# Performance work log

Hardware: AMD Instinct MI355X
Metric: run time of the kernel (lower is better)

The kernel has to match this reference:

```python
import jax, jax.numpy as jnp
import numpy as np

N, E = 50000, 600000
D_IN = 128; D_HID = 128; D_OUT = 128
HEADS = 4; HD = D_HID // HEADS  # per-head dim (32); also edge-encoder output dim
EDGE_DIM = 64


def _w(key, shape, scale=0.05):
    return jax.random.normal(key, shape, dtype=jnp.float32) * scale


def setup_inputs() -> dict:
    key = jax.random.key(0)
    ks = jax.random.split(key, 20)
    return {
        "x": jax.random.normal(ks[0], (N, D_IN), dtype=jnp.float32),
        "edge_index": jax.random.randint(ks[1], (2, E), 0, N),
        "edge_attr": jax.random.normal(ks[2], (E, EDGE_DIM), dtype=jnp.float32),
        # edge feature encoders: Linear(EDGE_DIM, HD), one per GNN layer
        "ew0": _w(ks[3], (EDGE_DIM, HD)), "eb0": jnp.zeros((HD,), jnp.float32),
        "ew1": _w(ks[4], (EDGE_DIM, HD)), "eb1": jnp.zeros((HD,), jnp.float32),
        # ordered-message-passing attention: Linear(dim, 1) per layer
        "ow0": _w(ks[5], (D_IN, 1)), "ob0": jnp.zeros((1,), jnp.float32),
        "ow1": _w(ks[6], (D_OUT, 1)), "ob1": jnp.zeros((1,), jnp.float32),
        # GATConv layer 0: in=D_IN, heads=HEADS, per-head out=HD, edge_dim=HD
        "g0_W": _w(ks[7], (D_IN, HEADS * HD)),
        "g0_as": _w(ks[8], (HEADS, HD)), "g0_ad": _w(ks[9], (HEADS, HD)),
        "g0_We": _w(ks[10], (HD, HEADS * HD)), "g0_ae": _w(ks[11], (HEADS, HD)),
        "g0_b": jnp.zeros((HEADS * HD,), jnp.float32),
        # GATConv layer 1 (final): in=HEADS*HD, heads=1, out=D_OUT, edge_dim=HD
        "g1_W": _w(ks[12], (HEADS * HD, D_OUT)),
        "g1_as": _w(ks[13], (1, D_OUT)), "g1_ad": _w(ks[14], (1, D_OUT)),
        "g1_We": _w(ks[15], (HD, D_OUT)), "g1_ae": _w(ks[16], (1, D_OUT)),
        "g1_b": jnp.zeros((D_OUT,), jnp.float32),
    }


def _gat_conv(x, src, dst, e_attr, W, a_src, a_dst, We, a_e, bias):
    """PyG GATConv with edge features, add_self_loops=True, fill_value='mean'."""
    H, C = a_src.shape
    n = x.shape[0]
    # self-loop edge_attr = per-dst mean of incoming edge_attr (PyG fill_value='mean')
    ones = jnp.ones((src.shape[0],), x.dtype)
    cnt = jax.ops.segment_sum(ones, dst, num_segments=n)
    loop_attr = jax.ops.segment_sum(e_attr, dst, num_segments=n) / jnp.maximum(cnt, 1.0)[:, None]
    loop = jnp.arange(n)
    src2 = jnp.concatenate([src, loop])
    dst2 = jnp.concatenate([dst, loop])
    ea2 = jnp.concatenate([e_attr, loop_attr], axis=0)  # [E+N, HD]
    xs = (x @ W).reshape(n, H, C)                       # [N, H, C]
    al_src = jnp.einsum('nhc,hc->nh', xs, a_src)
    al_dst = jnp.einsum('nhc,hc->nh', xs, a_dst)
    ee = (ea2 @ We).reshape(-1, H, C)                   # [E+N, H, C]
    al_e = jnp.einsum('ehc,hc->eh', ee, a_e)
    alpha = jax.nn.leaky_relu(al_src[src2] + al_dst[dst2] + al_e, 0.2)  # [E+N, H]
    # segment softmax over edges sharing a destination node
    mx = jax.ops.segment_max(alpha, dst2, num_segments=n)
    ex = jnp.exp(alpha - mx[dst2])
    den = jax.ops.segment_sum(ex, dst2, num_segments=n)
    coef = ex / (den[dst2] + 1e-16)
    out = jax.ops.segment_sum(xs[src2] * coef[..., None], dst2, num_segments=n)
    return out.reshape(n, H * C) + bias


def reference(x, edge_index, edge_attr, ew0, eb0, ew1, eb1, ow0, ob0, ow1, ob1,
              g0_W, g0_as, g0_ad, g0_We, g0_ae, g0_b,
              g1_W, g1_as, g1_ad, g1_We, g1_ae, g1_b):
    src, dst = edge_index[0], edge_index[1]
    original_x = x
    layers = [
        (ew0, eb0, ow0, ob0, g0_W, g0_as, g0_ad, g0_We, g0_ae, g0_b),
        (ew1, eb1, ow1, ob1, g1_W, g1_as, g1_ad, g1_We, g1_ae, g1_b),
    ]
    for i, (ew, eb, ow, ob, W, a_s, a_d, We, a_e, b) in enumerate(layers):
        te = jax.nn.relu(edge_attr @ ew + eb)            # [E, HD]
        score = (x @ ow + ob)[:, 0]                       # [N] order-attention scores
        te = te * jnp.exp(score)[src][:, None]            # ordered message weighting
        x_new = _gat_conv(x, src, dst, te, W, a_s, a_d, We, a_e, b)
        x = x_new + x if x.shape[-1] == x_new.shape[-1] else x_new
        if i < len(layers) - 1:
            x = jax.nn.relu(x)  # dropout p=0.0 in eval
    if original_x.shape[-1] == x.shape[-1]:
        x = x + original_x
    return x
```

## Files before the change

### kernel.cpp

```cpp
#include <hip/hip_runtime.h>
#include <math.h>

#define D 128
#define ED 64
#define HD 32

typedef short s16x8 __attribute__((ext_vector_type(8)));
typedef float f32x4 __attribute__((ext_vector_type(4)));

static __device__ inline unsigned short f2b(float f) {
  unsigned int u = __float_as_uint(f);
  unsigned int r = (u + 0x7fff + ((u >> 16) & 1)) >> 16;
  return (unsigned short)r;
}
static __device__ inline float b2f(unsigned short b) {
  return __uint_as_float(((unsigned int)b) << 16);
}

__global__ __launch_bounds__(256)
void count_prep_kernel(const int* __restrict__ dst, int* __restrict__ cnt, int E, int egrid,
                       const float* __restrict__ g0W, unsigned short* __restrict__ Wt0,
                       const float* __restrict__ g1W, unsigned short* __restrict__ Wt1,
                       const float* __restrict__ ew0, unsigned short* __restrict__ ewt0,
                       const float* __restrict__ ew1, unsigned short* __restrict__ ewt1,
                       const float* __restrict__ g0We, const float* __restrict__ g0ae,
                       float* __restrict__ M0,
                       const float* __restrict__ g1We, const float* __restrict__ g1ae,
                       float* __restrict__ M1) {
  int b = blockIdx.x, t = threadIdx.x;
  if (b < egrid) {
    int e = b * 256 + t;
    if (e < E) atomicAdd(&cnt[dst[e]], 1);
    return;
  }
  int pb = b - egrid;
  if (pb < 128) {
    const float* W = pb < 64 ? g0W : g1W;
    unsigned short* Wt = pb < 64 ? Wt0 : Wt1;
    int id = (pb & 63) * 256 + t;
    int nn = id >> 7, k = id & 127;
    Wt[id] = f2b(W[k * D + nn]);
  } else if (pb < 144) {
    const float* ew = pb < 136 ? ew0 : ew1;
    unsigned short* ewt = pb < 136 ? ewt0 : ewt1;
    int id = ((pb - 128) & 7) * 256 + t;
    if (id < HD * ED) {
      int i = id >> 6, k = id & 63;
      int ch = (i < 16) ? ((i >> 2) * 8 + (i & 3))
                        : (((i - 16) >> 2) * 8 + 4 + ((i - 16) & 3));
      ewt[id] = f2b(ew[k * HD + ch]);
    }
  } else if (pb == 144) {
    if (t < HD * 4) {
      int d = t >> 2, h = t & 3;
      float s = 0.f;
      for (int c = 0; c < 32; ++c) s += g0We[d * D + h * 32 + c] * g0ae[h * 32 + c];
      M0[t] = s;
    }
  } else {
    if (t < HD) {
      float s = 0.f;
      for (int c = 0; c < D; ++c) s += g1We[t * D + c] * g1ae[c];
      M1[t] = s;
    }
  }
}

__global__ __launch_bounds__(256)
void scan_a_kernel(const int* __restrict__ cnt, int* __restrict__ bsum, int n) {
  __shared__ int sh[256];
  int t = threadIdx.x;
  int i = blockIdx.x * 256 + t;
  sh[t] = (i < n) ? cnt[i] : 0;
  __syncthreads();
  for (int off = 128; off >= 1; off >>= 1) {
    if (t < off) sh[t] += sh[t + off];
    __syncthreads();
  }
  if (t == 0) bsum[blockIdx.x] = sh[0];
}

__global__ __launch_bounds__(256)
void scan_b_kernel(const int* __restrict__ bsum, int* __restrict__ boff, int nb,
                   int* __restrict__ rowptr_n, int E) {
  __shared__ int sh[256];
  int t = threadIdx.x;
  int v = (t < nb) ? bsum[t] : 0;
  sh[t] = v;
  __syncthreads();
  for (int off = 1; off < 256; off <<= 1) {
    int add = (t >= off) ? sh[t - off] : 0;
    __syncthreads();
    sh[t] += add;
    __syncthreads();
  }
  if (t < nb) boff[t] = sh[t] - v;
  if (t == 0) *rowptr_n = E;
}

__global__ __launch_bounds__(256)
void scan_c_kernel(const int* __restrict__ cnt, const int* __restrict__ boff,
                   int* __restrict__ rowptr, int n) {
  __shared__ int sh[256];
  int t = threadIdx.x;
  int i = blockIdx.x * 256 + t;
  int v = (i < n) ? cnt[i] : 0;
  sh[t] = v;
  __syncthreads();
  for (int off = 1; off < 256; off <<= 1) {
    int add = (t >= off) ? sh[t - off] : 0;
    __syncthreads();
    sh[t] += add;
    __syncthreads();
  }
  if (i < n) rowptr[i] = boff[blockIdx.x] + sh[t] - v;
}

template<int H>
static __device__ void gemm_body(int gblk, int tid,
                                 const float* __restrict__ x,
                                 const unsigned short* __restrict__ Wt,
                                 const float* __restrict__ a_s, const float* __restrict__ a_d,
                                 const float* __restrict__ ow, const float* __restrict__ ob,
                                 unsigned short* __restrict__ xs, float* __restrict__ al_src,
                                 float* __restrict__ al_dst, float* __restrict__ escore,
                                 float2* __restrict__ als1, int n) {
  int wave = tid >> 6;
  int lane = tid & 63;
  int q = lane >> 4;
  int l16 = lane & 15;
  int base = gblk * 64 + wave * 16;
  int rowRaw = base + l16;
  int row = rowRaw < n ? rowRaw : n - 1;
  const float* xrow = x + (size_t)row * D;
  s16x8 a[4];
  float scp = 0.f;
#pragma unroll
  for (int kk = 0; kk < 4; ++kk) {
    int kb = kk * 32 + q * 8;
    float4 v0 = *(const float4*)(xrow + kb);
    float4 v1 = *(const float4*)(xrow + kb + 4);
    float4 o0 = *(const float4*)(ow + kb);
    float4 o1 = *(const float4*)(ow + kb + 4);
    scp += v0.x * o0.x + v0.y * o0.y + v0.z * o0.z + v0.w * o0.w
         + v1.x * o1.x + v1.y * o1.y + v1.z * o1.z + v1.w * o1.w;
    s16x8 t;
    t[0] = (short)f2b(v0.x); t[1] = (short)f2b(v0.y);
    t[2] = (short)f2b(v0.z); t[3] = (short)f2b(v0.w);
    t[4] = (short)f2b(v1.x); t[5] = (short)f2b(v1.y);
    t[6] = (short)f2b(v1.z); t[7] = (short)f2b(v1.w);
    a[kk] = t;
  }
  scp += __shfl_xor(scp, 16);
  scp += __shfl_xor(scp, 32);
  if (H == 4) {
    if (q == 0 && rowRaw < n) escore[rowRaw] = __expf(scp + ob[0]);
  }

  f32x4 acc[8];
#pragma unroll
  for (int nf = 0; nf < 8; ++nf) { f32x4 z = {0.f, 0.f, 0.f, 0.f}; acc[nf] = z; }
#pragma unroll
  for (int kk = 0; kk < 4; ++kk) {
    int kb = kk * 32 + q * 8;
#pragma unroll
    for (int nf = 0; nf < 8; ++nf) {
      s16x8 b = *(const s16x8*)(Wt + (size_t)(nf * 16 + l16) * D + kb);
      acc[nf] = __builtin_amdgcn_mfma_f32_16x16x32_bf16(a[kk], b, acc[nf], 0, 0, 0);
    }
  }
#pragma unroll
  for (int nf = 0; nf < 8; ++nf) {
#pragma unroll
    for (int r = 0; r < 4; ++r) {
      int rr = base + q * 4 + r;
      if (rr < n) xs[(size_t)rr * D + nf * 16 + l16] = f2b(acc[nf][r]);
    }
  }
  float asv[8], adv[8];
#pragma unroll
  for (int nf = 0; nf < 8; ++nf) { asv[nf] = a_s[nf * 16 + l16]; adv[nf] = a_d[nf * 16 + l16]; }
  if (H == 4) {
    float mys = 0.f, myd = 0.f;
#pragma unroll
    for (int r = 0; r < 4; ++r) {
#pragma unroll
      for (int h = 0; h < 4; ++h) {
        float vs = acc[2 * h][r] * asv[2 * h] + acc[2 * h + 1][r] * asv[2 * h + 1];
        float vd = acc[2 * h][r] * adv[2 * h] + acc[2 * h + 1][r] * adv[2 * h + 1];
        vs += __shfl_xor(vs, 1); vd += __shfl_xor(vd, 1);
        vs += __shfl_xor(vs, 2); vd += __shfl_xor(vd, 2);
        vs += __shfl_xor(vs, 4); vd += __shfl_xor(vd, 4);
        vs += __shfl_xor(vs, 8); vd += __shfl_xor(vd, 8);
        if (l16 == r * 4 + h) { mys = vs; myd = vd; }
      }
    }
    int orow = base + q * 4 + (l16 >> 2);
    if (orow < n) {
      al_src[(size_t)orow * 4 + (l16 & 3)] = mys;
      al_dst[(size_t)orow * 4 + (l16 & 3)] = myd;
    }
  } else {
    float mys = 0.f, myd = 0.f;
#pragma unroll
    for (int r = 0; r < 4; ++r) {
      float vs = 0.f, vd = 0.f;
#pragma unroll
      for (int nf = 0; nf < 8; ++nf) { vs = fmaf(acc[nf][r], asv[nf], vs); vd = fmaf(acc[nf][r], adv[nf], vd); }
      vs += __shfl_xor(vs, 1); vd += __shfl_xor(vd, 1);
      vs += __shfl_xor(vs, 2); vd += __shfl_xor(vd, 2);
      vs += __shfl_xor(vs, 4); vd += __shfl_xor(vd, 4);
      vs += __shfl_xor(vs, 8); vd += __shfl_xor(vd, 8);
      if (l16 == r) { mys = vs; myd = vd; }
    }
    float scr = __shfl(scp, q * 4 + l16);
    int orow = base + q * 4 + l16;
    if (l16 < 4 && orow < n) {
      al_dst[orow] = myd;
      als1[orow] = make_float2(mys, __expf(scr + ob[0]));
    }
  }
}

__global__ __launch_bounds__(256)
void fill_gemm_kernel(const int* __restrict__ src, const int* __restrict__ dst,
                      const int* __restrict__ rowptr, int* __restrict__ cursor,
                      int2* __restrict__ slotmap, int E, int fgrid,
                      const float* __restrict__ x, const unsigned short* __restrict__ Wt0,
                      const float* __restrict__ g0as, const float* __restrict__ g0ad,
                      const float* __restrict__ ow0, const float* __restrict__ ob0,
                      unsigned short* __restrict__ xs, float* __restrict__ al_src,
                      float* __restrict__ al_dst, float* __restrict__ escore, int n) {
  if ((int)blockIdx.x < fgrid) {
    int e = blockIdx.x * 256 + threadIdx.x;
    if (e < E) {
      int d = dst[e];
      int p = atomicAdd(&cursor[d], 1);
      slotmap[rowptr[d] + p] = make_int2(e, src[e]);
    }
  } else {
    gemm_body<4>(blockIdx.x - fgrid, threadIdx.x, x, Wt0, g0as, g0ad, ow0, ob0,
                 xs, al_src, al_dst, escore, nullptr, n);
  }
}

__global__ __launch_bounds__(256)
void gemm1_kernel(const float* __restrict__ x, const unsigned short* __restrict__ Wt,
                  const float* __restrict__ a_s, const float* __restrict__ a_d,
                  const float* __restrict__ ow, const float* __restrict__ ob,
                  unsigned short* __restrict__ xs, float* __restrict__ al_dst,
                  float2* __restrict__ als1, int n) {
  gemm_body<1>(blockIdx.x, threadIdx.x, x, Wt, a_s, a_d, ow, ob,
               xs, nullptr, al_dst, nullptr, als1, n);
}

__global__ __launch_bounds__(256)
void edge_csr_kernel(const int2* __restrict__ slotmap,
                     const float* __restrict__ ea,
                     const unsigned short* __restrict__ ewt0p,
                     const unsigned short* __restrict__ ewt1p,
                     const float* __restrict__ eb0, const float* __restrict__ eb1,
                     const float* __restrict__ M0, const float* __restrict__ M1,
                     const float* __restrict__ escore0,
                     float* __restrict__ alef0,
                     float* __restrict__ ale1raw,
                     int E) {
  int wave = threadIdx.x >> 6, lane = threadIdx.x & 63;
  int q = lane >> 4, l16 = lane & 15;
  int ebase = (blockIdx.x * 4 + wave) * 64;
  if (ebase >= E) return;
  s16x8 a0l0 = *(const s16x8*)(ewt0p + l16 * 64 + q * 8);
  s16x8 a0l1 = *(const s16x8*)(ewt0p + l16 * 64 + 32 + q * 8);
  s16x8 a0h0 = *(const s16x8*)(ewt0p + (16 + l16) * 64 + q * 8);
  s16x8 a0h1 = *(const s16x8*)(ewt0p + (16 + l16) * 64 + 32 + q * 8);
  s16x8 a1l0 = *(const s16x8*)(ewt1p + l16 * 64 + q * 8);
  s16x8 a1l1 = *(const s16x8*)(ewt1p + l16 * 64 + 32 + q * 8);
  s16x8 a1h0 = *(const s16x8*)(ewt1p + (16 + l16) * 64 + q * 8);
  s16x8 a1h1 = *(const s16x8*)(ewt1p + (16 + l16) * 64 + 32 + q * 8);
  float4 b0lo = *(const float4*)(eb0 + q * 8);
  float4 b0hi = *(const float4*)(eb0 + q * 8 + 4);
  float4 b1lo = *(const float4*)(eb1 + q * 8);
  float4 b1hi = *(const float4*)(eb1 + q * 8 + 4);
  s16x8 mf0, mf1;
#pragma unroll
  for (int j = 0; j < 8; ++j) {
    mf0[j] = (l16 < 4) ? (short)f2b(M0[(q * 8 + j) * 4 + l16]) : (short)0;
    mf1[j] = (l16 == 0) ? (short)f2b(M1[q * 8 + j]) : (short)0;
  }
  int el = ebase + lane;
  int elc = el < E ? el : E - 1;
  int2 sm = slotmap[elc];
  int eo = sm.x;
  float esc = escore0[sm.y];

#pragma unroll
  for (int st = 0; st < 4; ++st) {
    int slot16 = st * 16 + l16;
    int e16 = ebase + slot16;
    int row = __shfl(eo, slot16);
    const float* er = ea + (size_t)row * ED;
    float4 u0 = *(const float4*)(er + q * 8);
    float4 u1 = *(const float4*)(er + q * 8 + 4);
    float4 u2 = *(const float4*)(er + 32 + q * 8);
    float4 u3 = *(const float4*)(er + 32 + q * 8 + 4);
    s16x8 bk0, bk1;
    bk0[0] = (short)f2b(u0.x); bk0[1] = (short)f2b(u0.y);
    bk0[2] = (short)f2b(u0.z); bk0[3] = (short)f2b(u0.w);
    bk0[4] = (short)f2b(u1.x); bk0[5] = (short)f2b(u1.y);
    bk0[6] = (short)f2b(u1.z); bk0[7] = (short)f2b(u1.w);
    bk1[0] = (short)f2b(u2.x); bk1[1] = (short)f2b(u2.y);
    bk1[2] = (short)f2b(u2.z); bk1[3] = (short)f2b(u2.w);
    bk1[4] = (short)f2b(u3.x); bk1[5] = (short)f2b(u3.y);
    bk1[6] = (short)f2b(u3.z); bk1[7] = (short)f2b(u3.w);
    f32x4 zl0 = {0.f,0.f,0.f,0.f}, zh0 = {0.f,0.f,0.f,0.f};
    f32x4 zl1 = {0.f,0.f,0.f,0.f}, zh1 = {0.f,0.f,0.f,0.f};
    zl0 = __builtin_amdgcn_mfma_f32_16x16x32_bf16(a0l0, bk0, zl0, 0, 0, 0);
    zl0 = __builtin_amdgcn_mfma_f32_16x16x32_bf16(a0l1, bk1, zl0, 0, 0, 0);
    zh0 = __builtin_amdgcn_mfma_f32_16x16x32_bf16(a0h0, bk0, zh0, 0, 0, 0);
    zh0 = __builtin_amdgcn_mfma_f32_16x16x32_bf16(a0h1, bk1, zh0, 0, 0, 0);
    zl1 = __builtin_amdgcn_mfma_f32_16x16x32_bf16(a1l0, bk0, zl1, 0, 0, 0);
    zl1 = __builtin_amdgcn_mfma_f32_16x16x32_bf16(a1l1, bk1, zl1, 0, 0, 0);
    zh1 = __builtin_amdgcn_mfma_f32_16x16x32_bf16(a1h0, bk0, zh1, 0, 0, 0);
    zh1 = __builtin_amdgcn_mfma_f32_16x16x32_bf16(a1h1, bk1, zh1, 0, 0, 0);
    s16x8 zb0, zb1;
    zb0[0] = (short)f2b(fmaxf(zl0[0] + b0lo.x, 0.f));
    zb0[1] = (short)f2b(fmaxf(zl0[1] + b0lo.y, 0.f));
    zb0[2] = (short)f2b(fmaxf(zl0[2] + b0lo.z, 0.f));
    zb0[3] = (short)f2b(fmaxf(zl0[3] + b0lo.w, 0.f));
    zb0[4] = (short)f2b(fmaxf(zh0[0] + b0hi.x, 0.f));
    zb0[5] = (short)f2b(fmaxf(zh0[1] + b0hi.y, 0.f));
    zb0[6] = (short)f2b(fmaxf(zh0[2] + b0hi.z, 0.f));
    zb0[7] = (short)f2b(fmaxf(zh0[3] + b0hi.w, 0.f));
    zb1[0] = (short)f2b(fmaxf(zl1[0] + b1lo.x, 0.f));
    zb1[1] = (short)f2b(fmaxf(zl1[1] + b1lo.y, 0.f));
    zb1[2] = (short)f2b(fmaxf(zl1[2] + b1lo.z, 0.f));
    zb1[3] = (short)f2b(fmaxf(zl1[3] + b1lo.w, 0.f));
    zb1[4] = (short)f2b(fmaxf(zh1[0] + b1hi.x, 0.f));
    zb1[5] = (short)f2b(fmaxf(zh1[1] + b1hi.y, 0.f));
    zb1[6] = (short)f2b(fmaxf(zh1[2] + b1hi.z, 0.f));
    zb1[7] = (short)f2b(fmaxf(zh1[3] + b1hi.w, 0.f));
    f32x4 r0 = {0.f,0.f,0.f,0.f}, r1 = {0.f,0.f,0.f,0.f};
    r0 = __builtin_amdgcn_mfma_f32_16x16x32_bf16(mf0, zb0, r0, 0, 0, 0);
    r1 = __builtin_amdgcn_mfma_f32_16x16x32_bf16(mf1, zb1, r1, 0, 0, 0);
    float esc_e = __shfl(esc, slot16);
    if (q == 0 && e16 < E) {
      *(float4*)(alef0 + (size_t)e16 * 4) =
          make_float4(r0[0] * esc_e, r0[1] * esc_e, r0[2] * esc_e, r0[3] * esc_e);
      ale1raw[e16] = r1[0];
    }
  }
}

template<int H, bool RELU, bool ADD_ORIG>
__global__ __launch_bounds__(256)
void agg_kernel(const int* __restrict__ rowptr, const int2* __restrict__ slotmap,
                const unsigned short* __restrict__ xs, const float* __restrict__ alef,
                const float* __restrict__ al_src, const float* __restrict__ al_dst,
                const float2* __restrict__ als1,
                const float* __restrict__ bias, const float* __restrict__ xin,
                const float* __restrict__ orig, float* __restrict__ out, int n) {
  int wid = blockIdx.x * 4 + (threadIdx.x >> 6);
  int lane = threadIdx.x & 63;
  if (wid >= n) return;
  int half = lane >> 5;
  int l32 = lane & 31;
  int h0 = (H == 4) ? (l32 >> 3) : 0;
  const ushort4* xs4 = (const ushort4*)xs;
  float adst = al_dst[(size_t)wid * H + h0];
  float ax0 = 0.f, ax1 = 0.f, ax2 = 0.f, ax3 = 0.f, den = 0.f, sale = 0.f;
  int b = rowptr[wid], e = rowptr[wid + 1];
  int m = e - b;

#define EDGE_ACC(I_)                                                     \
  {                                                                      \
    int s_ = slotmap[I_].y;                                              \
    float al_, ev_;                                                      \
    if (H == 4) {                                                        \
      al_ = alef[(size_t)(I_) * 4 + h0];                                 \
      float aa_ = al_src[(size_t)s_ * 4 + h0] + adst + al_;              \
      ev_ = __expf(aa_ > 0.f ? aa_ : 0.2f * aa_);                        \
    } else {                                                             \
      float2 ae_ = als1[s_];                                             \
      al_ = alef[I_] * ae_.y;                                            \
      float aa_ = ae_.x + adst + al_;                                    \
      ev_ = __expf(aa_ > 0.f ? aa_ : 0.2f * aa_);                        \
    }                                                                    \
    ushort4 u_ = xs4[(size_t)s_ * 32 + l32];                             \
    ax0 = fmaf(ev_, b2f(u_.x), ax0); ax1 = fmaf(ev_, b2f(u_.y), ax1);    \
    ax2 = fmaf(ev_, b2f(u_.z), ax2); ax3 = fmaf(ev_, b2f(u_.w), ax3);    \
    den += ev_; sale += al_;                                             \
  }

  int k = 0;
  for (; k + 8 <= m; k += 8) {
    int i0 = b + k + half;
    EDGE_ACC(i0)
    EDGE_ACC(i0 + 2)
    EDGE_ACC(i0 + 4)
    EDGE_ACC(i0 + 6)
  }
  for (int idx = b + k + half; idx < e; idx += 2) EDGE_ACC(idx)
#undef EDGE_ACC

  ax0 += __shfl_xor(ax0, 32); ax1 += __shfl_xor(ax1, 32);
  ax2 += __shfl_xor(ax2, 32); ax3 += __shfl_xor(ax3, 32);
  den += __shfl_xor(den, 32); sale += __shfl_xor(sale, 32);

  float la = sale / (float)(m > 1 ? m : 1);
  float asrc_w = (H == 4) ? al_src[(size_t)wid * 4 + h0] : als1[wid].x;
  float a = asrc_w + adst + la;
  float lr = a > 0.f ? a : 0.2f * a;
  float evl = __expf(lr);
  ushort4 us = xs4[(size_t)wid * 32 + l32];
  ax0 = fmaf(evl, b2f(us.x), ax0); ax1 = fmaf(evl, b2f(us.y), ax1);
  ax2 = fmaf(evl, b2f(us.z), ax2); ax3 = fmaf(evl, b2f(us.w), ax3);
  float dinv = 1.f / (den + evl + 1e-16f);
  if (half == 0) {
    float4 bi = ((const float4*)bias)[l32];
    float4 xi = ((const float4*)xin)[(size_t)wid * 32 + l32];
    float4 o;
    o.x = ax0 * dinv + bi.x + xi.x;
    o.y = ax1 * dinv + bi.y + xi.y;
    o.z = ax2 * dinv + bi.z + xi.z;
    o.w = ax3 * dinv + bi.w + xi.w;
    if (ADD_ORIG) {
      float4 og = ((const float4*)orig)[(size_t)wid * 32 + l32];
      o.x += og.x; o.y += og.y; o.z += og.z; o.w += og.w;
    }
    if (RELU) {
      o.x = fmaxf(o.x, 0.f); o.y = fmaxf(o.y, 0.f);
      o.z = fmaxf(o.z, 0.f); o.w = fmaxf(o.w, 0.f);
    }
    ((float4*)out)[(size_t)wid * 32 + l32] = o;
  }
}

extern "C" void kernel_launch(void* const* d_in, const int* in_sizes, int n_in,
                              void* d_out, int out_size, void* d_ws, size_t ws_size,
                              hipStream_t stream) {
  const float* x   = (const float*)d_in[0];
  const int*   ei  = (const int*)d_in[1];
  const float* ea  = (const float*)d_in[2];
  const float* ew0 = (const float*)d_in[3];
  const float* eb0 = (const float*)d_in[4];
  const float* ew1 = (const float*)d_in[5];
  const float* eb1 = (const float*)d_in[6];
  const float* ow0 = (const float*)d_in[7];
  const float* ob0 = (const float*)d_in[8];
  const float* ow1 = (const float*)d_in[9];
  const float* ob1 = (const float*)d_in[10];
  const float* g0W = (const float*)d_in[11];
  const float* g0as= (const float*)d_in[12];
  const float* g0ad= (const float*)d_in[13];
  const float* g0We= (const float*)d_in[14];
  const float* g0ae= (const float*)d_in[15];
  const float* g0b = (const float*)d_in[16];
  const float* g1W = (const float*)d_in[17];
  const float* g1as= (const float*)d_in[18];
  const float* g1ad= (const float*)d_in[19];
  const float* g1We= (const float*)d_in[20];
  const float* g1ae= (const float*)d_in[21];
  const float* g1b = (const float*)d_in[22];
  float* out = (float*)d_out;

  const int N = in_sizes[0] / D;
  const int E = in_sizes[1] / 2;
  const int* srcp = ei;
  const int* dstp = ei + E;

  char* w = (char*)d_ws;
  size_t off = 0;
  auto alloc = [&](size_t bytes) {
    void* p = w + off;
    off += (bytes + 255) & ~(size_t)255;
    return p;
  };
  size_t Nb = ((size_t)N * 4 + 255) & ~(size_t)255;
  int*   cnt     = (int*)alloc(2 * Nb);
  int*   cursor  = (int*)((char*)cnt + Nb);
  unsigned short* xs = (unsigned short*)alloc((size_t)N * D * 2);
  float* alef0   = (float*)alloc((size_t)E * 4 * 4);
  float* ale1raw = (float*)alloc((size_t)E * 4);
  float* al_src  = (float*)alloc((size_t)N * 4 * 4);
  float* al_dst  = (float*)alloc((size_t)N * 4 * 4);
  float* escore  = (float*)alloc((size_t)N * 4);
  float2* als1   = (float2*)alloc((size_t)N * 8);
  float* M0      = (float*)alloc(HD * 4 * 4);
  float* M1      = (float*)alloc(HD * 4);
  unsigned short* Wt0 = (unsigned short*)alloc((size_t)D * D * 2);
  unsigned short* Wt1 = (unsigned short*)alloc((size_t)D * D * 2);
  unsigned short* ewt0 = (unsigned short*)alloc((size_t)HD * ED * 2);
  unsigned short* ewt1 = (unsigned short*)alloc((size_t)HD * ED * 2);
  int*   rowptr  = (int*)alloc((size_t)(N + 1) * 4);
  int2*  slotmap = (int2*)alloc((size_t)E * 8);
  int*   bsum    = (int*)alloc(1024);
  int*   boff    = (int*)alloc(1024);

  int egrid  = (E + 255) / 256;
  int ngrid4 = (N + 3) / 4;
  int ggrid  = (N + 63) / 64;
  int nsb    = (N + 255) / 256;

  hipMemsetAsync(cnt, 0, 2 * Nb, stream);
  count_prep_kernel<<<egrid + 146, 256, 0, stream>>>(dstp, cnt, E, egrid,
                                                     g0W, Wt0, g1W, Wt1,
                                                     ew0, ewt0, ew1, ewt1,
                                                     g0We, g0ae, M0, g1We, g1ae, M1);
  scan_a_kernel<<<nsb, 256, 0, stream>>>(cnt, bsum, N);
  scan_b_kernel<<<1, 256, 0, stream>>>(bsum, boff, nsb, rowptr + N, E);
  scan_c_kernel<<<nsb, 256, 0, stream>>>(cnt, boff, rowptr, N);
  fill_gemm_kernel<<<egrid + ggrid, 256, 0, stream>>>(srcp, dstp, rowptr, cursor,
                                                      slotmap, E, egrid,
                                                      x, Wt0, g0as, g0ad, ow0, ob0,
                                                      xs, al_src, al_dst, escore, N);
  edge_csr_kernel<<<egrid, 256, 0, stream>>>(slotmap, ea, ewt0, ewt1,
                                             eb0, eb1, M0, M1, escore,
                                             alef0, ale1raw, E);
  agg_kernel<4, true, false><<<ngrid4, 256, 0, stream>>>(rowptr, slotmap,
                                                         xs, alef0,
                                                         al_src, al_dst, nullptr,
                                                         g0b, x, nullptr, out, N);
  gemm1_kernel<<<ggrid, 256, 0, stream>>>(out, Wt1, g1as, g1ad, ow1, ob1,
                                          xs, al_dst, als1, N);
  agg_kernel<1, false, true><<<ngrid4, 256, 0, stream>>>(rowptr, slotmap,
                                                         xs, ale1raw,
                                                         nullptr, al_dst, als1,
                                                         g1b, out, x, out, N);
}
```

Baseline: 241.8 us.

## Store layer-0 output in bf16 and widen aggregation gathers to 16-byte loads

The intermediate layer-0 activation is now written as bf16 into a separate buffer, which gemm1 and the final aggregation read instead of the fp32 output. This halves that tensor's traffic and skips the fp32-to-bf16 conversion in gemm1. The aggregation kernel also changes its lane mapping so each lane gathers 8 bf16 values (16 bytes) and the wave handles 4 edges at once instead of 2. That means fewer, wider gathers, at the cost of more registers and an extra shuffle stage. The residual add now uses the rounded bf16 value, which slightly reduces precision.

Measured after the change: 251.2 us. 1.04x slower.

```diff
diff --git a/kernel.cpp b/kernel.cpp
--- a/kernel.cpp
+++ b/kernel.cpp
@@ -6,6 +6,7 @@
 #define HD 32
 
 typedef short s16x8 __attribute__((ext_vector_type(8)));
+typedef unsigned short u16x8 __attribute__((ext_vector_type(8)));
 typedef float f32x4 __attribute__((ext_vector_type(4)));
 
 static __device__ inline unsigned short f2b(float f) {
@@ -116,9 +117,8 @@
   if (i < n) rowptr[i] = boff[blockIdx.x] + sh[t] - v;
 }
 
-template<int H>
-static __device__ void gemm_body(int gblk, int tid,
-                                 const float* __restrict__ x,
+template<int H, bool INBF16>
+static __device__ void gemm_body(int gblk, int tid, const void* xin,
                                  const unsigned short* __restrict__ Wt,
                                  const float* __restrict__ a_s, const float* __restrict__ a_d,
                                  const float* __restrict__ ow, const float* __restrict__ ob,
@@ -132,24 +132,38 @@
   int base = gblk * 64 + wave * 16;
   int rowRaw = base + l16;
   int row = rowRaw < n ? rowRaw : n - 1;
-  const float* xrow = x + (size_t)row * D;
   s16x8 a[4];
   float scp = 0.f;
-#pragma unroll
-  for (int kk = 0; kk < 4; ++kk) {
-    int kb = kk * 32 + q * 8;
-    float4 v0 = *(const float4*)(xrow + kb);
-    float4 v1 = *(const float4*)(xrow + kb + 4);
-    float4 o0 = *(const float4*)(ow + kb);
-    float4 o1 = *(const float4*)(ow + kb + 4);
-    scp += v0.x * o0.x + v0.y * o0.y + v0.z * o0.z + v0.w * o0.w
-         + v1.x * o1.x + v1.y * o1.y + v1.z * o1.z + v1.w * o1.w;
-    s16x8 t;
-    t[0] = (short)f2b(v0.x); t[1] = (short)f2b(v0.y);
-    t[2] = (short)f2b(v0.z); t[3] = (short)f2b(v0.w);
-    t[4] = (short)f2b(v1.x); t[5] = (short)f2b(v1.y);
-    t[6] = (short)f2b(v1.z); t[7] = (short)f2b(v1.w);
-    a[kk] = t;
+  if (INBF16) {
+    const unsigned short* xrow = (const unsigned short*)xin + (size_t)row * D;
+#pragma unroll
+    for (int kk = 0; kk < 4; ++kk) {
+      int kb = kk * 32 + q * 8;
+      u16x8 v = *(const u16x8*)(xrow + kb);
+      float4 o0 = *(const float4*)(ow + kb);
+      float4 o1 = *(const float4*)(ow + kb + 4);
+      scp += b2f(v[0]) * o0.x + b2f(v[1]) * o0.y + b2f(v[2]) * o0.z + b2f(v[3]) * o0.w
+           + b2f(v[4]) * o1.x + b2f(v[5]) * o1.y + b2f(v[6]) * o1.z + b2f(v[7]) * o1.w;
+      a[kk] = *(const s16x8*)&v;
+    }
+  } else {
+    const float* xrow = (const float*)xin + (size_t)row * D;
+#pragma unroll
+    for (int kk = 0; kk < 4; ++kk) {
+      int kb = kk * 32 + q * 8;
+      float4 v0 = *(const float4*)(xrow + kb);
+      float4 v1 = *(const float4*)(xrow + kb + 4);
+      float4 o0 = *(const float4*)(ow + kb);
+      float4 o1 = *(const float4*)(ow + kb + 4);
+      scp += v0.x * o0.x + v0.y * o0.y + v0.z * o0.z + v0.w * o0.w
+           + v1.x * o1.x + v1.y * o1.y + v1.z * o1.z + v1.w * o1.w;
+      s16x8 t;
+      t[0] = (short)f2b(v0.x); t[1] = (short)f2b(v0.y);
+      t[2] = (short)f2b(v0.z); t[3] = (short)f2b(v0.w);
+      t[4] = (short)f2b(v1.x); t[5] = (short)f2b(v1.y);
+      t[6] = (short)f2b(v1.z); t[7] = (short)f2b(v1.w);
+      a[kk] = t;
+    }
   }
   scp += __shfl_xor(scp, 16);
   scp += __shfl_xor(scp, 32);
@@ -239,19 +253,19 @@
       slotmap[rowptr[d] + p] = make_int2(e, src[e]);
     }
   } else {
-    gemm_body<4>(blockIdx.x - fgrid, threadIdx.x, x, Wt0, g0as, g0ad, ow0, ob0,
-                 xs, al_src, al_dst, escore, nullptr, n);
-  }
-}
-
-__global__ __launch_bounds__(256)
-void gemm1_kernel(const float* __restrict__ x, const unsigned short* __restrict__ Wt,
+    gemm_body<4, false>(blockIdx.x - fgrid, threadIdx.x, x, Wt0, g0as, g0ad, ow0, ob0,
+                        xs, al_src, al_dst, escore, nullptr, n);
+  }
+}
+
+__global__ __launch_bounds__(256)
+void gemm1_kernel(const unsigned short* __restrict__ x1b, const unsigned short* __restrict__ Wt,
                   const float* __restrict__ a_s, const float* __restrict__ a_d,
                   const float* __restrict__ ow, const float* __restrict__ ob,
                   unsigned short* __restrict__ xs, float* __restrict__ al_dst,
                   float2* __restrict__ als1, int n) {
-  gemm_body<1>(blockIdx.x, threadIdx.x, x, Wt, a_s, a_d, ow, ob,
-               xs, nullptr, al_dst, nullptr, als1, n);
+  gemm_body<1, true>(blockIdx.x, threadIdx.x, x1b, Wt, a_s, a_d, ow, ob,
+                     xs, nullptr, al_dst, nullptr, als1, n);
 }
 
 __global__ __launch_bounds__(256)
@@ -351,23 +365,26 @@
   }
 }
 
-template<int H, bool RELU, bool ADD_ORIG>
+template<int H, bool RELU, bool ADD_ORIG, bool INBF16, bool OUTBF16>
 __global__ __launch_bounds__(256)
 void agg_kernel(const int* __restrict__ rowptr, const int2* __restrict__ slotmap,
                 const unsigned short* __restrict__ xs, const float* __restrict__ alef,
                 const float* __restrict__ al_src, const float* __restrict__ al_dst,
                 const float2* __restrict__ als1,
-                const float* __restrict__ bias, const float* __restrict__ xin,
-                const float* __restrict__ orig, float* __restrict__ out, int n) {
+                const float* __restrict__ bias, const void* __restrict__ xin,
+                const float* __restrict__ orig, void* __restrict__ outv, int n) {
   int wid = blockIdx.x * 4 + (threadIdx.x >> 6);
   int lane = threadIdx.x & 63;
   if (wid >= n) return;
-  int half = lane >> 5;
-  int l32 = lane & 31;
-  int h0 = (H == 4) ? (l32 >> 3) : 0;
-  const ushort4* xs4 = (const ushort4*)xs;
+  int q2 = lane >> 4;
+  int l16 = lane & 15;
+  int h0 = (H == 4) ? (l16 >> 2) : 0;
+  const u16x8* xs8 = (const u16x8*)xs;
   float adst = al_dst[(size_t)wid * H + h0];
-  float ax0 = 0.f, ax1 = 0.f, ax2 = 0.f, ax3 = 0.f, den = 0.f, sale = 0.f;
+  float ax[8];
+#pragma unroll
+  for (int j = 0; j < 8; ++j) ax[j] = 0.f;
+  float den = 0.f, sale = 0.f;
   int b = rowptr[wid], e = rowptr[wid + 1];
   int m = e - b;
 
@@ -385,53 +402,80 @@
       float aa_ = ae_.x + adst + al_;                                    \
       ev_ = __expf(aa_ > 0.f ? aa_ : 0.2f * aa_);                        \
     }                                                                    \
-    ushort4 u_ = xs4[(size_t)s_ * 32 + l32];                             \
-    ax0 = fmaf(ev_, b2f(u_.x), ax0); ax1 = fmaf(ev_, b2f(u_.y), ax1);    \
-    ax2 = fmaf(ev_, b2f(u_.z), ax2); ax3 = fmaf(ev_, b2f(u_.w), ax3);    \
+    u16x8 u_ = xs8[(size_t)s_ * 16 + l16];                               \
+    _Pragma("unroll")                                                    \
+    for (int j = 0; j < 8; ++j) ax[j] = fmaf(ev_, b2f(u_[j]), ax[j]);    \
     den += ev_; sale += al_;                                             \
   }
 
   int k = 0;
-  for (; k + 8 <= m; k += 8) {
-    int i0 = b + k + half;
+  for (; k + 16 <= m; k += 16) {
+    int i0 = b + k + q2;
     EDGE_ACC(i0)
-    EDGE_ACC(i0 + 2)
     EDGE_ACC(i0 + 4)
-    EDGE_ACC(i0 + 6)
-  }
-  for (int idx = b + k + half; idx < e; idx += 2) EDGE_ACC(idx)
+    EDGE_ACC(i0 + 8)
+    EDGE_ACC(i0 + 12)
+  }
+  for (int idx = b + k + q2; idx < e; idx += 4) EDGE_ACC(idx)
 #undef EDGE_ACC
 
-  ax0 += __shfl_xor(ax0, 32); ax1 += __shfl_xor(ax1, 32);
-  ax2 += __shfl_xor(ax2, 32); ax3 += __shfl_xor(ax3, 32);
-  den += __shfl_xor(den, 32); sale += __shfl_xor(sale, 32);
+#pragma unroll
+  for (int j = 0; j < 8; ++j) {
+    ax[j] += __shfl_xor(ax[j], 16);
+    ax[j] += __shfl_xor(ax[j], 32);
+  }
+  den += __shfl_xor(den, 16); den += __shfl_xor(den, 32);
+  sale += __shfl_xor(sale, 16); sale += __shfl_xor(sale, 32);
 
   float la = sale / (float)(m > 1 ? m : 1);
   float asrc_w = (H == 4) ? al_src[(size_t)wid * 4 + h0] : als1[wid].x;
   float a = asrc_w + adst + la;
   float lr = a > 0.f ? a : 0.2f * a;
   float evl = __expf(lr);
-  ushort4 us = xs4[(size_t)wid * 32 + l32];
-  ax0 = fmaf(evl, b2f(us.x), ax0); ax1 = fmaf(evl, b2f(us.y), ax1);
-  ax2 = fmaf(evl, b2f(us.z), ax2); ax3 = fmaf(evl, b2f(us.w), ax3);
+  u16x8 us = xs8[(size_t)wid * 16 + l16];
+#pragma unroll
+  for (int j = 0; j < 8; ++j) ax[j] = fmaf(evl, b2f(us[j]), ax[j]);
   float dinv = 1.f / (den + evl + 1e-16f);
-  if (half == 0) {
-    float4 bi = ((const float4*)bias)[l32];
-    float4 xi = ((const float4*)xin)[(size_t)wid * 32 + l32];
-    float4 o;
-    o.x = ax0 * dinv + bi.x + xi.x;
-    o.y = ax1 * dinv + bi.y + xi.y;
-    o.z = ax2 * dinv + bi.z + xi.z;
-    o.w = ax3 * dinv + bi.w + xi.w;
+  if (q2 == 0) {
+    float o[8];
+    float4 bi0 = *(const float4*)(bias + l16 * 8);
+    float4 bi1 = *(const float4*)(bias + l16 * 8 + 4);
+    o[0] = ax[0] * dinv + bi0.x; o[1] = ax[1] * dinv + bi0.y;
+    o[2] = ax[2] * dinv + bi0.z; o[3] = ax[3] * dinv + bi0.w;
+    o[4] = ax[4] * dinv + bi1.x; o[5] = ax[5] * dinv + bi1.y;
+    o[6] = ax[6] * dinv + bi1.z; o[7] = ax[7] * dinv + bi1.w;
+    if (INBF16) {
+      u16x8 xi = ((const u16x8*)xin)[(size_t)wid * 16 + l16];
+#pragma unroll
+      for (int j = 0; j < 8; ++j) o[j] += b2f(xi[j]);
+    } else {
+      const float* xf = (const float*)xin + (size_t)wid * D + l16 * 8;
+      float4 x0 = *(const float4*)xf;
+      float4 x1 = *(const float4*)(xf + 4);
+      o[0] += x0.x; o[1] += x0.y; o[2] += x0.z; o[3] += x0.w;
+      o[4] += x1.x; o[5] += x1.y; o[6] += x1.z; o[7] += x1.w;
+    }
     if (ADD_ORIG) {
-      float4 og = ((const float4*)orig)[(size_t)wid * 32 + l32];
-      o.x += og.x; o.y += og.y; o.z += og.z; o.w += og.w;
+      const float* og = orig + (size_t)wid * D + l16 * 8;
+      float4 g0 = *(const float4*)og;
+      float4 g1 = *(const float4*)(og + 4);
+      o[0] += g0.x; o[1] += g0.y; o[2] += g0.z; o[3] += g0.w;
+      o[4] += g1.x; o[5] += g1.y; o[6] += g1.z; o[7] += g1.w;
     }
     if (RELU) {
-      o.x = fmaxf(o.x, 0.f); o.y = fmaxf(o.y, 0.f);
-      o.z = fmaxf(o.z, 0.f); o.w = fmaxf(o.w, 0.f);
-    }
-    ((float4*)out)[(size_t)wid * 32 + l32] = o;
+#pragma unroll
+      for (int j = 0; j < 8; ++j) o[j] = fmaxf(o[j], 0.f);
+    }
+    if (OUTBF16) {
+      u16x8 ob;
+#pragma unroll
+      for (int j = 0; j < 8; ++j) ob[j] = f2b(o[j]);
+      ((u16x8*)outv)[(size_t)wid * 16 + l16] = ob;
+    } else {
+      float* of = (float*)outv + (size_t)wid * D + l16 * 8;
+      *(float4*)of = make_float4(o[0], o[1], o[2], o[3]);
+      *(float4*)(of + 4) = make_float4(o[4], o[5], o[6], o[7]);
+    }
   }
 }
 
@@ -478,7 +522,8 @@
   size_t Nb = ((size_t)N * 4 + 255) & ~(size_t)255;
   int*   cnt     = (int*)alloc(2 * Nb);
   int*   cursor  = (int*)((char*)cnt + Nb);
-  unsigned short* xs = (unsigned short*)alloc((size_t)N * D * 2);
+  unsigned short* xs   = (unsigned short*)alloc((size_t)N * D * 2);
+  unsigned short* x1b  = (unsigned short*)alloc((size_t)N * D * 2);
   float* alef0   = (float*)alloc((size_t)E * 4 * 4);
   float* ale1raw = (float*)alloc((size_t)E * 4);
   float* al_src  = (float*)alloc((size_t)N * 4 * 4);
@@ -516,14 +561,12 @@
   edge_csr_kernel<<<egrid, 256, 0, stream>>>(slotmap, ea, ewt0, ewt1,
                                              eb0, eb1, M0, M1, escore,
                                              alef0, ale1raw, E);
-  agg_kernel<4, true, false><<<ngrid4, 256, 0, stream>>>(rowptr, slotmap,
-                                                         xs, alef0,
-                                                         al_src, al_dst, nullptr,
-                                                         g0b, x, nullptr, out, N);
-  gemm1_kernel<<<ggrid, 256, 0, stream>>>(out, Wt1, g1as, g1ad, ow1, ob1,
+  agg_kernel<4, true, false, false, true><<<ngrid4, 256, 0, stream>>>(
+      rowptr, slotmap, xs, alef0, al_src, al_dst, nullptr,
+      g0b, x, nullptr, x1b, N);
+  gemm1_kernel<<<ggrid, 256, 0, stream>>>(x1b, Wt1, g1as, g1ad, ow1, ob1,
                                           xs, al_dst, als1, N);
-  agg_kernel<1, false, true><<<ngrid4, 256, 0, stream>>>(rowptr, slotmap,
-                                                         xs, ale1raw,
-                                                         nullptr, al_dst, als1,
-                                                         g1b, out, x, out, N);
-}
+  agg_kernel<1, false, true, true, false><<<ngrid4, 256, 0, stream>>>(
+      rowptr, slotmap, xs, ale1raw, nullptr, al_dst, als1,
+      g1b, x1b, x, out, N);
+}
```
